# Performance work log

Hardware: AMD Instinct MI355X
Metric: run time of the kernel (lower is better)

Reference implementation:

```python
import jax, jax.numpy as jnp
import numpy as np

EPS = 1e-12  # F.normalize default eps
SCALE = 8 * 56  # magic denominator from the original code


def setup_inputs() -> dict:
    key = jax.random.key(0)
    B, C, K = 256, 2048, 4
    P = B // K  # 64 identities
    k1, k2 = jax.random.split(key)
    inputs = jax.random.normal(k1, (B, C), dtype=jnp.float32)
    # PK-sampled batch: P identities, each with K=4 consecutive samples
    targets = jnp.repeat(jnp.arange(P, dtype=jnp.int32), K)
    # binary modality label (visible / infrared)
    subs = jax.random.randint(k2, (B,), 0, 2, dtype=jnp.int32)
    return {"inputs": inputs, "targets": targets, "subs": subs}


def reference(inputs, targets, subs):
    B, C = inputs.shape
    # centers[i] = mean of samples sharing identity targets[4*i]
    center_t = targets[::4]                                  # (P,)
    cmask = (targets[None, :] == center_t[:, None]).astype(inputs.dtype)  # (P, B)
    centers = (cmask @ inputs) / cmask.sum(-1, keepdims=True)             # (P, C)

    id_mask = targets[None, :] == targets[:, None]           # (B, B) bool
    # modality_mask = subs[None,:] == subs[:,None]  # computed but unused in original

    def per_center(c):
        vec = inputs - c                                     # (B, C)
        vec = vec / jnp.maximum(
            jnp.linalg.norm(vec, axis=-1, keepdims=True), EPS)
        angle = vec @ vec.T                                  # (B, B) cosine angles
        # min over positives per row (each row has exactly 4 positives)
        pos = jnp.where(id_mask, angle, jnp.inf).min(axis=-1)            # (B,)
        # max over clamp(angle, 0) on negatives per row
        neg = jnp.where(id_mask, 0.0, jnp.maximum(angle, 0.0)).max(axis=-1)
        # matmul(exp(-pos).T, exp(neg)) is a (1,1) dot product; .mean() is identity
        return jnp.sum(jnp.exp(-pos) * jnp.exp(neg)) / SCALE

    losses = jax.vmap(per_center)(centers)                   # (P,)
    # NOTE: original returns `loss` (the LAST iteration's loss), not the
    # accumulated `losses` — we reproduce that behavior faithfully.
    return losses[-1]
```

## Files before the change

kernel.cpp:

```cpp
#include <hip/hip_runtime.h>
#include <math.h>

#define BN 256
#define CN 2048
#define C4 512
#define EPSF 1e-12f

__global__ __launch_bounds__(256, 1) void gram_kernel(const float* __restrict__ in,
                                                      float* __restrict__ D,
                                                      float* __restrict__ s_pre,
                                                      float* __restrict__ out) {
    const int b   = blockIdx.x;
    const int ib  = b >> 3;
    const int jb  = b & 7;
    const int tid = threadIdx.x;

    if (32 * jb + 31 < 4 * ib) {
        if (b == 64 && tid == 0) out[0] = 0.f;
        return;
    }

    const int i0   = ib * 4;
    const int j0   = jb * 32;
    const int lane = tid & 63;
    const int wave = tid >> 6;
    const bool odd1 = (lane & 1);
    const bool odd2 = (lane & 2);

    __shared__ float s_ctr[16];

    const float4* __restrict__ in4 = (const float4*)in;

    float4 a[4][8];
#pragma unroll
    for (int r = 0; r < 4; ++r)
#pragma unroll
        for (int t = 0; t < 8; ++t)
            a[r][t] = in4[(i0 + r) * C4 + lane + 64 * t];

#pragma unroll 2
    for (int s = 0; s < 8; ++s) {
        const int j = j0 + wave + 4 * s;
        float4 bv[8];
#pragma unroll
        for (int t = 0; t < 8; ++t)
            bv[t] = in4[j * C4 + lane + 64 * t];

        float a0 = 0.f, a1 = 0.f, a2 = 0.f, a3 = 0.f;
#pragma unroll
        for (int t = 0; t < 8; ++t) {
            const float4 b4 = bv[t];
            a0 += a[0][t].x * b4.x + a[0][t].y * b4.y + a[0][t].z * b4.z + a[0][t].w * b4.w;
            a1 += a[1][t].x * b4.x + a[1][t].y * b4.y + a[1][t].z * b4.z + a[1][t].w * b4.w;
            a2 += a[2][t].x * b4.x + a[2][t].y * b4.y + a[2][t].z * b4.z + a[2][t].w * b4.w;
            a3 += a[3][t].x * b4.x + a[3][t].y * b4.y + a[3][t].z * b4.z + a[3][t].w * b4.w;
        }

        const float c01 = (odd1 ? a1 : a0) + __shfl_xor(odd1 ? a0 : a1, 1, 64);
        const float c23 = (odd1 ? a3 : a2) + __shfl_xor(odd1 ? a2 : a3, 1, 64);
        float c = (odd2 ? c23 : c01) + __shfl_xor(odd2 ? c01 : c23, 2, 64);
        c += __shfl_xor(c, 4, 64);
        c += __shfl_xor(c, 8, 64);
        c += __shfl_xor(c, 16, 64);
        c += __shfl_xor(c, 32, 64);

        if (lane < 4) {
            const int i = i0 + lane;
            D[i * BN + j] = c;
            D[j * BN + i] = c;
            if (jb == 7 && s == 7)
                s_ctr[wave * 4 + lane] = c;
        }
    }

    if (jb == 7) {
        __syncthreads();
        if (tid < 4) {
            const float sp = (((s_ctr[tid] + s_ctr[4 + tid]) + s_ctr[8 + tid])
                              + s_ctr[12 + tid]) * 0.25f;
            s_pre[i0 + tid] = sp;
        }
    }
}

__global__ __launch_bounds__(256) void finish_kernel(const float* __restrict__ D,
                                                     const float* __restrict__ s_pre,
                                                     const int* __restrict__ targets,
                                                     float* __restrict__ out) {
    const int tid = threadIdx.x;
    const int blk = blockIdx.x;

    __shared__ int   s_t[BN];
    __shared__ float s_s[BN];
    __shared__ float s_inv[BN];
    __shared__ float s_red[4];

    const int row = blk * 32 + (tid >> 3);
    const int sub = tid & 7;

    const float4* __restrict__ D4 = (const float4*)D;
    float4 drow[8];
#pragma unroll
    for (int q = 0; q < 8; ++q)
        drow[q] = D4[row * (BN / 4) + q * 8 + sub];

    const int   t_own = targets[tid];
    const float dii   = D[tid * BN + tid];
    const float si    = s_pre[tid];
    const int   ti    = targets[row];
    const float diiR  = D[row * BN + row];
    const float siR   = s_pre[row];
    const float sp0   = s_pre[BN - 4];
    const float sp1   = s_pre[BN - 3];
    const float sp2   = s_pre[BN - 2];
    const float sp3   = s_pre[BN - 1];

    const float cc = (((sp0 + sp1) + sp2) + sp3) * 0.25f;

    const float nrm2 = fmaxf(dii - 2.f * si + cc, 0.f);
    const float inv  = 1.0f / fmaxf(sqrtf(nrm2), EPSF);
    const float nrm2R = fmaxf(diiR - 2.f * siR + cc, 0.f);
    const float invR  = 1.0f / fmaxf(sqrtf(nrm2R), EPSF);

    s_t[tid]   = t_own;
    s_s[tid]   = si;
    s_inv[tid] = inv;
    __syncthreads();

    float pos = INFINITY;
    float neg = 0.f;
#pragma unroll
    for (int q = 0; q < 8; ++q) {
        const float4 d = drow[q];
        const int j = 4 * (q * 8 + sub);
        const float g0 = (d.x - siR - s_s[j + 0] + cc) * invR * s_inv[j + 0];
        const float g1 = (d.y - siR - s_s[j + 1] + cc) * invR * s_inv[j + 1];
        const float g2 = (d.z - siR - s_s[j + 2] + cc) * invR * s_inv[j + 2];
        const float g3 = (d.w - siR - s_s[j + 3] + cc) * invR * s_inv[j + 3];
        if (s_t[j + 0] == ti) pos = fminf(pos, g0); else neg = fmaxf(neg, fmaxf(g0, 0.f));
        if (s_t[j + 1] == ti) pos = fminf(pos, g1); else neg = fmaxf(neg, fmaxf(g1, 0.f));
        if (s_t[j + 2] == ti) pos = fminf(pos, g2); else neg = fmaxf(neg, fmaxf(g2, 0.f));
        if (s_t[j + 3] == ti) pos = fminf(pos, g3); else neg = fmaxf(neg, fmaxf(g3, 0.f));
    }
#pragma unroll
    for (int off = 1; off <= 4; off <<= 1) {
        pos = fminf(pos, __shfl_xor(pos, off, 64));
        neg = fmaxf(neg, __shfl_xor(neg, off, 64));
    }
    float val = (sub == 0) ? expf(neg - pos) : 0.f;
#pragma unroll
    for (int off = 1; off <= 32; off <<= 1) val += __shfl_xor(val, off, 64);
    if ((tid & 63) == 0) s_red[tid >> 6] = val;
    __syncthreads();
    if (tid == 0)
        atomicAdd(out, (s_red[0] + s_red[1] + s_red[2] + s_red[3]) * (1.0f / 448.0f));
}

extern "C" void kernel_launch(void* const* d_in, const int* in_sizes, int n_in,
                              void* d_out, int out_size, void* d_ws, size_t ws_size,
                              hipStream_t stream) {
    const float* in      = (const float*)d_in[0];
    const int*   targets = (const int*)d_in[1];

    float* D     = (float*)d_ws;
    float* s_pre = D + BN * BN;
    float* out   = (float*)d_out;

    gram_kernel  <<<512, 256, 0, stream>>>(in, D, s_pre, out);
    finish_kernel<<<8,   256, 0, stream>>>(D, s_pre, targets, out);
}
```

Baseline: 70.79 us.

## Balance Gram work across 256 blocks with flattened triangular work units

Replaces the 512-block launch, where many blocks exited early on the lower triangle, with 256 blocks that each handle 9 consecutive (tile, s) work units decoded from a flattened triangular index. A-tile registers are reloaded only when the row block changes. This removes idle early-exit blocks and evens out per-block work, but adds index decoding and a block-wide sync inside the loop when a unit finishes a center tile.

```diff
diff --git a/kernel.cpp b/kernel.cpp
--- a/kernel.cpp
+++ b/kernel.cpp
@@ -10,50 +10,56 @@
                                                       float* __restrict__ D,
                                                       float* __restrict__ s_pre,
                                                       float* __restrict__ out) {
-    const int b   = blockIdx.x;
-    const int ib  = b >> 3;
-    const int jb  = b & 7;
-    const int tid = threadIdx.x;
-
-    if (32 * jb + 31 < 4 * ib) {
-        if (b == 64 && tid == 0) out[0] = 0.f;
-        return;
-    }
-
-    const int i0   = ib * 4;
-    const int j0   = jb * 32;
+    const int b    = blockIdx.x;
+    const int tid  = threadIdx.x;
     const int lane = tid & 63;
     const int wave = tid >> 6;
     const bool odd1 = (lane & 1);
     const bool odd2 = (lane & 2);
+
+    if (b == 0 && tid == 0) out[0] = 0.f;
 
     __shared__ float s_ctr[16];
 
     const float4* __restrict__ in4 = (const float4*)in;
 
     float4 a[4][8];
+    int cur_ib = -1;
+
+    const int u0 = 9 * b;
+    for (int k = 0; k < 9; ++k) {
+        const int u = u0 + k;
+        const int t = u >> 3;
+        const int s = u & 7;
+        int jb = 0;
+        jb += (t >= 8);   jb += (t >= 24);  jb += (t >= 48);  jb += (t >= 80);
+        jb += (t >= 120); jb += (t >= 168); jb += (t >= 224);
+        const int ib = t - 4 * jb * (jb + 1);
+        const int i0 = ib * 4;
+
+        if (ib != cur_ib) {
+            cur_ib = ib;
 #pragma unroll
-    for (int r = 0; r < 4; ++r)
+            for (int r = 0; r < 4; ++r)
 #pragma unroll
-        for (int t = 0; t < 8; ++t)
-            a[r][t] = in4[(i0 + r) * C4 + lane + 64 * t];
+                for (int tt = 0; tt < 8; ++tt)
+                    a[r][tt] = in4[(i0 + r) * C4 + lane + 64 * tt];
+        }
 
-#pragma unroll 2
-    for (int s = 0; s < 8; ++s) {
-        const int j = j0 + wave + 4 * s;
+        const int j = 32 * jb + wave + 4 * s;
         float4 bv[8];
 #pragma unroll
-        for (int t = 0; t < 8; ++t)
-            bv[t] = in4[j * C4 + lane + 64 * t];
+        for (int tt = 0; tt < 8; ++tt)
+            bv[tt] = in4[j * C4 + lane + 64 * tt];
 
         float a0 = 0.f, a1 = 0.f, a2 = 0.f, a3 = 0.f;
 #pragma unroll
-        for (int t = 0; t < 8; ++t) {
-            const float4 b4 = bv[t];
-            a0 += a[0][t].x * b4.x + a[0][t].y * b4.y + a[0][t].z * b4.z + a[0][t].w * b4.w;
-            a1 += a[1][t].x * b4.x + a[1][t].y * b4.y + a[1][t].z * b4.z + a[1][t].w * b4.w;
-            a2 += a[2][t].x * b4.x + a[2][t].y * b4.y + a[2][t].z * b4.z + a[2][t].w * b4.w;
-            a3 += a[3][t].x * b4.x + a[3][t].y * b4.y + a[3][t].z * b4.z + a[3][t].w * b4.w;
+        for (int tt = 0; tt < 8; ++tt) {
+            const float4 b4 = bv[tt];
+            a0 += a[0][tt].x * b4.x + a[0][tt].y * b4.y + a[0][tt].z * b4.z + a[0][tt].w * b4.w;
+            a1 += a[1][tt].x * b4.x + a[1][tt].y * b4.y + a[1][tt].z * b4.z + a[1][tt].w * b4.w;
+            a2 += a[2][tt].x * b4.x + a[2][tt].y * b4.y + a[2][tt].z * b4.z + a[2][tt].w * b4.w;
+            a3 += a[3][tt].x * b4.x + a[3][tt].y * b4.y + a[3][tt].z * b4.z + a[3][tt].w * b4.w;
         }
 
         const float c01 = (odd1 ? a1 : a0) + __shfl_xor(odd1 ? a0 : a1, 1, 64);
@@ -71,14 +77,15 @@
             if (jb == 7 && s == 7)
                 s_ctr[wave * 4 + lane] = c;
         }
-    }
 
-    if (jb == 7) {
-        __syncthreads();
-        if (tid < 4) {
-            const float sp = (((s_ctr[tid] + s_ctr[4 + tid]) + s_ctr[8 + tid])
-                              + s_ctr[12 + tid]) * 0.25f;
-            s_pre[i0 + tid] = sp;
+        if (jb == 7 && s == 7) {
+            __syncthreads();
+            if (tid < 4) {
+                const float sp = (((s_ctr[tid] + s_ctr[4 + tid]) + s_ctr[8 + tid])
+                                  + s_ctr[12 + tid]) * 0.25f;
+                s_pre[i0 + tid] = sp;
+            }
+            __syncthreads();
         }
     }
 }
@@ -166,6 +173,6 @@
     float* s_pre = D + BN * BN;
     float* out   = (float*)d_out;
 
-    gram_kernel  <<<512, 256, 0, stream>>>(in, D, s_pre, out);
+    gram_kernel  <<<256, 256, 0, stream>>>(in, D, s_pre, out);
     finish_kernel<<<8,   256, 0, stream>>>(D, s_pre, targets, out);
 }
```

After: 72.94 us. 3.0% more time.
